# Performance work log

Measured on AMD Instinct MI355X. Metric: run time of the kernel, lower is better.

The kernel has to match this reference:

```python
import jax, jax.numpy as jnp
import numpy as np

D = 200          # in_feat == out_feat
N = 20000        # num nodes
E = 320000       # num edges
R = 512          # num relation types


def setup_inputs() -> dict:
    key = jax.random.key(0)
    ks = jax.random.split(key, 12)
    # glorot-ish init scale for params
    def glorot(k, shape):
        fan = shape[0] + shape[1]
        return jax.random.normal(k, shape, dtype=jnp.float32) * jnp.sqrt(2.0 / fan)
    return {
        "node": jax.random.normal(ks[0], (N, D), dtype=jnp.float32),
        "rel": jax.random.normal(ks[1], (R, D), dtype=jnp.float32),
        "norm": jax.random.uniform(ks[2], (N, 1), dtype=jnp.float32),
        "fre": jax.random.uniform(ks[3], (E,), dtype=jnp.float32),
        "w_triplet": glorot(ks[4], (3 * D, D)),
        "w_quad": glorot(ks[5], (D, D)),
        "loop_weight": glorot(ks[6], (D, D)),
        "evolve_loop_weight": glorot(ks[7], (D, D)),
        "edge_src": jax.random.randint(ks[8], (E,), 0, N, dtype=jnp.int64).astype(jnp.int32),
        "edge_dst": jax.random.randint(ks[9], (E,), 0, N, dtype=jnp.int64).astype(jnp.int32),
        "edge_type": jax.random.randint(ks[10], (E,), 0, R, dtype=jnp.int64).astype(jnp.int32),
    }


def reference(node, rel, norm, fre, w_triplet, w_quad, loop_weight,
              evolve_loop_weight, edge_src, edge_dst, edge_type):
    n = node.shape[0]
    d = node.shape[1]
    # gather per-edge features
    src_h = node[edge_src]            # [E, D]
    dst_h = node[edge_dst]            # [E, D]
    rel_emb = rel[edge_type]          # [E, D]
    # quads_msg_func: concat([src,rel,dst]) @ w_triplet, split to avoid [E,3D] concat
    W_s, W_r, W_d = w_triplet[:d], w_triplet[d:2 * d], w_triplet[2 * d:]
    triplet = src_h @ W_s + rel_emb @ W_r + dst_h @ W_d   # [E, D]
    a = (triplet + fre[:, None]) @ w_quad                 # [E, D]
    a = jax.nn.leaky_relu(a, negative_slope=0.01)
    # edge softmax over incoming edges per destination node (per channel)
    seg_max = jax.ops.segment_max(a, edge_dst, num_segments=n)   # [N, D]
    ex = jnp.exp(a - seg_max[edge_dst])
    seg_sum = jax.ops.segment_sum(ex, edge_dst, num_segments=n)  # [N, D]
    att = ex / seg_sum[edge_dst]
    # weighted message aggregation + per-node norm
    h = jax.ops.segment_sum(att * triplet, edge_dst, num_segments=n)
    h = h * norm
    # self-loop: loop_weight where in_degree > 0, else evolve_loop_weight
    deg = jax.ops.segment_sum(jnp.ones((edge_dst.shape[0],), dtype=jnp.float32),
                              edge_dst, num_segments=n)
    loop_msg = jnp.where((deg > 0)[:, None],
                         node @ loop_weight,
                         node @ evolve_loop_weight)
    return jax.nn.relu(h + loop_msg)
```

## Files before the change

### kernel.cpp

```cpp
#include <hip/hip_runtime.h>
#include <hip/hip_bf16.h>
#include <cstdint>
#include <cstddef>

#define DD 200
#define NN 20000
#define EE 320000
#define RRR 512
#define KP 256
#define KREAL 224
#define MT 157
#define NT 10
#define RMT 4
#define RNT 4
#define NBLK_NODE (MT * NT)

#define PB_NODE 10000
#define PB_REL  (PB_NODE + 256)
#define PB_HIST (PB_REL + 1250)
#define PB_W    (PB_HIST + 200)
#define PB_CQ   (PB_W + 1)
#define PB_PAD  (PB_CQ + 196)

typedef __attribute__((ext_vector_type(8))) short bf16x8;
typedef __attribute__((ext_vector_type(4))) float f32x4;

__device__ __forceinline__ float bf2f_lo(unsigned int u) { return __uint_as_float(u << 16); }
__device__ __forceinline__ float bf2f_hi(unsigned int u) { return __uint_as_float(u & 0xffff0000u); }
__device__ __forceinline__ unsigned short f2bf(float f) {
  unsigned int x = __float_as_uint(f);
  return (unsigned short)((x + 0x7fffu + ((x >> 16) & 1u)) >> 16);
}
__device__ __forceinline__ unsigned int f2bf2(float a, float b) {
  return (unsigned int)f2bf(a) | ((unsigned int)f2bf(b) << 16);
}
__device__ __forceinline__ void gl_lds16(const unsigned short* g, unsigned short* l) {
  __builtin_amdgcn_global_load_lds(
      (const __attribute__((address_space(1))) void*)g,
      (__attribute__((address_space(3))) void*)l, 16, 0, 0);
}

__global__ __launch_bounds__(256) void kPrep(const float* __restrict__ node, const float* __restrict__ rel,
                                             const int* __restrict__ dst,
                                             const float* __restrict__ wt, const float* __restrict__ wq,
                                             const float* __restrict__ lw, const float* __restrict__ elw,
                                             unsigned int* __restrict__ Au, unsigned int* __restrict__ Arelu,
                                             int* __restrict__ deg,
                                             unsigned short* __restrict__ Bt, unsigned short* __restrict__ BtRel,
                                             float* __restrict__ cq) {
  int b = blockIdx.x, t = threadIdx.x;
  if (b < PB_NODE) {
    int h = t >> 7, tt = t & 127;
    int n = b * 2 + h;
    unsigned v = 0;
    if (tt < 100) { float2 f = ((const float2*)(node + (size_t)n * DD))[tt]; v = f2bf2(f.x, f.y); }
    Au[(size_t)n * 128 + tt] = v;
  } else if (b < PB_REL) {
    int h = t >> 7, tt = t & 127;
    int r = (b - PB_NODE) * 2 + h;
    unsigned v = 0;
    if (tt < 100) { float2 f = ((const float2*)(rel + (size_t)r * DD))[tt]; v = f2bf2(f.x, f.y); }
    Arelu[(size_t)r * 128 + tt] = v;
  } else if (b < PB_HIST) {
    int e = (b - PB_REL) * 256 + t;
    if (e < EE) atomicAdd(&deg[dst[e]], 1);
  } else if (b < PB_W) {
    int k = b - PB_HIST, j = t;
    if (j >= DD) return;
    const float* w0 = wt + (size_t)k * DD;
    const float* w1 = wt + (size_t)(2 * DD + k) * DD;
    const float* w2 = wt + (size_t)(DD + k) * DD;
    float s0 = 0.f, s1 = 0.f, s2 = 0.f;
    for (int i = 0; i < DD; ++i) {
      float q = wq[i * DD + j];
      s0 = fmaf(w0[i], q, s0);
      s1 = fmaf(w1[i], q, s1);
      s2 = fmaf(w2[i], q, s2);
    }
    Bt[(2 * j) * KP + k]       = f2bf(w0[j]);
    Bt[(2 * j + 1) * KP + k]   = f2bf(s0);
    Bt[(400 + 2 * j) * KP + k] = f2bf(w1[j]);
    Bt[(401 + 2 * j) * KP + k] = f2bf(s1);
    Bt[(800 + 2 * j) * KP + k] = f2bf(lw[k * DD + j]);
    Bt[(801 + 2 * j) * KP + k] = f2bf(elw[k * DD + j]);
    BtRel[(2 * j) * KP + k]     = f2bf(w2[j]);
    BtRel[(2 * j + 1) * KP + k] = f2bf(s2);
  } else if (b < PB_CQ) {
    int j = t; if (j >= DD) return;
    float s = 0.f;
    for (int i = 0; i < DD; ++i) s += wq[i * DD + j];
    cq[j] = s;
  } else {
    int idx = (b - PB_CQ) * 256 + t;
    ((unsigned int*)Bt)[(idx / 28) * 128 + 100 + idx % 28] = 0;
  }
}

__global__ __launch_bounds__(1024) void k_scan(const int* __restrict__ deg, int* __restrict__ offs) {
  __shared__ int wsum[16];
  int tid = threadIdx.x, lane = tid & 63, wv = tid >> 6;
  const int4* deg4 = (const int4*)deg;
  int4* offs4 = (int4*)offs;
  int4 v[5]; int ps[5]; int tsum = 0;
#pragma unroll
  for (int c = 0; c < 5; ++c) {
    int idx = tid * 5 + c;
    v[c] = (idx < 5000) ? deg4[idx] : make_int4(0, 0, 0, 0);
    ps[c] = tsum;
    tsum += v[c].x + v[c].y + v[c].z + v[c].w;
  }
  int x = tsum;
#pragma unroll
  for (int off = 1; off < 64; off <<= 1) {
    int y = __shfl_up(x, off, 64);
    if (lane >= off) x += y;
  }
  if (lane == 63) wsum[wv] = x;
  __syncthreads();
  if (wv == 0) {
    int w = (lane < 16) ? wsum[lane] : 0;
#pragma unroll
    for (int off = 1; off < 16; off <<= 1) {
      int y = __shfl_up(w, off, 64);
      if (lane >= off) w += y;
    }
    if (lane < 16) wsum[lane] = w;
  }
  __syncthreads();
  int pre = ((wv > 0) ? wsum[wv - 1] : 0) + x - tsum;
#pragma unroll
  for (int c = 0; c < 5; ++c) {
    int idx = tid * 5 + c;
    if (idx < 5000) {
      int a = pre + ps[c];
      int bq = a + v[c].x, cc = bq + v[c].y, d = cc + v[c].z;
      offs4[idx] = make_int4(a, bq, cc, d);
    }
  }
  if (tid == 0) offs[NN] = wsum[15];
}

__global__ __launch_bounds__(256) void k_gemm(const unsigned short* __restrict__ A,
                                              const unsigned short* __restrict__ Bt,
                                              unsigned short* __restrict__ NT2u,
                                              const unsigned short* __restrict__ Arel,
                                              const unsigned short* __restrict__ BtRel,
                                              unsigned short* __restrict__ RelPu) {
  __shared__ unsigned short As[128 * 32];
  __shared__ unsigned short Bs[128 * 32];
  bool isrel = blockIdx.x >= NBLK_NODE;
  int bid, ntn;
  const unsigned short *Ag, *Bg;
  if (!isrel) { bid = blockIdx.x; ntn = NT; Ag = A; Bg = Bt; }
  else        { bid = blockIdx.x - NBLK_NODE; ntn = RNT; Ag = Arel; Bg = BtRel; }
  int mt = bid / ntn, nt = bid % ntn;
  int t = threadIdx.x, lane = t & 63, wv = t >> 6;
  int lr = lane & 15, k8 = lane >> 4;
  int wm = (wv >> 1) * 64, wn = (wv & 1) * 64;
  int sr = wv * 16 + (lane >> 2);
  int sc = lane & 3;
  f32x4 acc[4][4] = {};
  Ag += (size_t)(mt * 128) * KP;
  Bg += (size_t)(nt * 128) * KP;
  for (int kk = 0; kk < KREAL; kk += 32) {
#pragma unroll
    for (int i = 0; i < 2; ++i) {
      int row = i * 64 + sr;
      int gcol = kk + ((sc ^ (row & 3)) << 3);
      gl_lds16(Ag + (size_t)row * KP + gcol, As + i * 2048 + wv * 512);
      gl_lds16(Bg + (size_t)row * KP + gcol, Bs + i * 2048 + wv * 512);
    }
    __syncthreads();
    bf16x8 af[4], bfr[4];
#pragma unroll
    for (int mi = 0; mi < 4; ++mi) {
      int row = wm + mi * 16 + lr;
      af[mi] = *(const bf16x8*)(As + row * 32 + ((k8 ^ (row & 3)) << 3));
      int col = wn + mi * 16 + lr;
      bfr[mi] = *(const bf16x8*)(Bs + col * 32 + ((k8 ^ (col & 3)) << 3));
    }
#pragma unroll
    for (int mi = 0; mi < 4; ++mi)
#pragma unroll
      for (int ni = 0; ni < 4; ++ni)
        acc[mi][ni] = __builtin_amdgcn_mfma_f32_16x16x32_bf16(af[mi], bfr[ni], acc[mi][ni], 0, 0, 0);
    __syncthreads();
  }
  int rb = k8 * 4;
#pragma unroll
  for (int mi = 0; mi < 4; ++mi)
#pragma unroll
    for (int ni = 0; ni < 4; ++ni) {
      int col = nt * 128 + wn + ni * 16 + lr;
      if (!isrel) {
        if (col < 1200) {
          int g = col / 400, w = col - g * 400;
          unsigned short* dst = NT2u + (size_t)g * NN * 400 + w;
#pragma unroll
          for (int r = 0; r < 4; ++r) {
            int row = mt * 128 + wm + mi * 16 + rb + r;
            if (row < NN) dst[(size_t)row * 400] = f2bf(acc[mi][ni][r]);
          }
        }
      } else {
        if (col < 400) {
#pragma unroll
          for (int r = 0; r < 4; ++r) {
            int row = mt * 128 + wm + mi * 16 + rb + r;
            RelPu[(size_t)row * 400 + col] = f2bf(acc[mi][ni][r]);
          }
        }
      }
    }
}

__global__ __launch_bounds__(256) void k_scatter(const int* __restrict__ src, const int* __restrict__ dst,
                                                 const int* __restrict__ typ, const float* __restrict__ fre,
                                                 const int* __restrict__ offs, int* __restrict__ cursor,
                                                 int2* __restrict__ erec) {
  int e = blockIdx.x * 256 + threadIdx.x;
  if (e >= EE) return;
  int d = dst[e];
  int p = offs[d] + atomicAdd(&cursor[d], 1);
  erec[p] = make_int2(src[e] | (typ[e] << 15), __float_as_int(fre[e]));
}

__global__ __launch_bounds__(128) void k_agg(const uint2* __restrict__ GS2,
                                             const uint2* __restrict__ GD2,
                                             const uint2* __restrict__ GL2,
                                             const uint2* __restrict__ Rel2,
                                             const float2* __restrict__ cq2,
                                             const float* __restrict__ norm,
                                             const int* __restrict__ offs,
                                             const int2* __restrict__ erec,
                                             float* __restrict__ out) {
  int n = blockIdx.x;
  int j2 = threadIdx.x;
  if (j2 >= 100) return;
  int e0 = offs[n], e1 = offs[n + 1];
  uint2 dp = GD2[(size_t)n * 100 + j2];
  float xd0 = bf2f_lo(dp.x), xq0 = bf2f_hi(dp.x);
  float xd1 = bf2f_lo(dp.y), xq1 = bf2f_hi(dp.y);
  float2 cqv = cq2[j2];
  float s0 = 0.f, s1 = 0.f, num0 = 0.f, num1 = 0.f;
#define DO_EDGE(SP, RP, FI)                                                   \
  {                                                                           \
    float F = __int_as_float(FI);                                             \
    float t0 = bf2f_lo(SP.x) + bf2f_lo(RP.x);                                 \
    float a0 = bf2f_hi(SP.x) + bf2f_hi(RP.x) + fmaf(F, cqv.x, xq0);           \
    float t1 = bf2f_lo(SP.y) + bf2f_lo(RP.y);                                 \
    float a1 = bf2f_hi(SP.y) + bf2f_hi(RP.y) + fmaf(F, cqv.y, xq1);           \
    a0 = fmaxf(a0, 0.01f * a0); a1 = fmaxf(a1, 0.01f * a1);                   \
    float ev0 = __expf(a0), ev1 = __expf(a1);                                 \
    s0 += ev0; num0 = fmaf(ev0, t0, num0);                                    \
    s1 += ev1; num1 = fmaf(ev1, t1, num1);                                    \
  }
  int i = e0;
  for (; i + 8 <= e1; i += 8) {
    int2 r[8]; uint2 g[8], R[8];
#pragma unroll
    for (int u = 0; u < 8; ++u) r[u] = erec[i + u];
#pragma unroll
    for (int u = 0; u < 8; ++u) g[u] = GS2[((unsigned)r[u].x & 0x7fffu) * 100u + j2];
#pragma unroll
    for (int u = 0; u < 8; ++u) R[u] = Rel2[((unsigned)r[u].x >> 15) * 100u + j2];
#pragma unroll
    for (int u = 0; u < 8; ++u) DO_EDGE(g[u], R[u], r[u].y)
  }
  if (i + 4 <= e1) {
    int2 r[4]; uint2 g[4], R[4];
#pragma unroll
    for (int u = 0; u < 4; ++u) r[u] = erec[i + u];
#pragma unroll
    for (int u = 0; u < 4; ++u) g[u] = GS2[((unsigned)r[u].x & 0x7fffu) * 100u + j2];
#pragma unroll
    for (int u = 0; u < 4; ++u) R[u] = Rel2[((unsigned)r[u].x >> 15) * 100u + j2];
#pragma unroll
    for (int u = 0; u < 4; ++u) DO_EDGE(g[u], R[u], r[u].y)
    i += 4;
  }
  for (; i < e1; ++i) {
    int2 r = erec[i];
    uint2 g = GS2[((unsigned)r.x & 0x7fffu) * 100u + j2];
    uint2 R = Rel2[((unsigned)r.x >> 15) * 100u + j2];
    DO_EDGE(g, R, r.y)
  }
#undef DO_EDGE
  uint2 lp = GL2[(size_t)n * 100 + j2];
  float o0, o1;
  if (e1 > e0) {
    float nm = norm[n];
    o0 = (num0 / s0 + xd0) * nm + bf2f_lo(lp.x);
    o1 = (num1 / s1 + xd1) * nm + bf2f_lo(lp.y);
  } else {
    o0 = bf2f_hi(lp.x);
    o1 = bf2f_hi(lp.y);
  }
  ((float2*)(out + (size_t)n * DD))[j2] = make_float2(fmaxf(o0, 0.f), fmaxf(o1, 0.f));
}

extern "C" void kernel_launch(void* const* d_in, const int* in_sizes, int n_in,
                              void* d_out, int out_size, void* d_ws, size_t ws_size,
                              hipStream_t stream) {
  const float* node = (const float*)d_in[0];
  const float* rel  = (const float*)d_in[1];
  const float* norm = (const float*)d_in[2];
  const float* fre  = (const float*)d_in[3];
  const float* wt   = (const float*)d_in[4];
  const float* wq   = (const float*)d_in[5];
  const float* lw   = (const float*)d_in[6];
  const float* elw  = (const float*)d_in[7];
  const int* esrc = (const int*)d_in[8];
  const int* edst = (const int*)d_in[9];
  const int* etyp = (const int*)d_in[10];
  float* out = (float*)d_out;

  char* p = (char*)d_ws;
  auto carve = [&](size_t bytes) -> char* {
    char* r = p; p += (bytes + 255) & ~(size_t)255; return r;
  };
  unsigned short* A     = (unsigned short*)carve((size_t)(MT * 128) * KP * 2);
  unsigned short* Arel  = (unsigned short*)carve((size_t)RRR * KP * 2);
  unsigned short* BtAll = (unsigned short*)carve((size_t)(1280 + 512) * KP * 2);
  unsigned short* NT2   = (unsigned short*)carve((size_t)3 * NN * 400 * 2);
  unsigned short* RelP  = (unsigned short*)carve((size_t)RRR * 400 * 2);
  float* cq   = (float*)carve((size_t)DD * 4);
  int* degcur = (int*)carve((size_t)2 * NN * 4);
  int* offs   = (int*)carve((size_t)(NN + 1) * 4);
  int2* erec  = (int2*)carve((size_t)EE * 8);

  unsigned short* Bt    = BtAll;
  unsigned short* BtRel = BtAll + (size_t)1280 * KP;
  int* deg    = degcur;
  int* cursor = degcur + NN;

  const uint2* GS2 = (const uint2*)NT2;
  const uint2* GD2 = GS2 + (size_t)NN * 100;
  const uint2* GL2 = GS2 + (size_t)2 * NN * 100;

  hipMemsetAsync(degcur, 0, (size_t)2 * NN * 4, stream);
  kPrep<<<PB_PAD, 256, 0, stream>>>(node, rel, edst, wt, wq, lw, elw,
                                    (unsigned int*)A, (unsigned int*)Arel, deg, Bt, BtRel, cq);
  k_scan<<<1, 1024, 0, stream>>>(deg, offs);
  k_scatter<<<(EE + 255) / 256, 256, 0, stream>>>(esrc, edst, etyp, fre, offs, cursor, erec);
  k_gemm<<<NBLK_NODE + RMT * RNT, 256, 0, stream>>>(A, Bt, NT2, Arel, BtRel, RelP);
  k_agg<<<NN, 128, 0, stream>>>(GS2, GD2, GL2, (const uint2*)RelP, (const float2*)cq,
                                norm, offs, erec, out);
}
```

Baseline: 142.3 us.

## Merge scatter into GEMM launch, software-pipeline edge loads, fold log2e into weights

Moves the edge-scatter blocks into the same launch as the bf16 GEMM, so CSR record building overlaps with the matrix work and one kernel launch goes away. The log2(e) factor is folded into the attention-logit weight columns and cq, so the aggregation kernel can call exp2f instead of __expf. The per-node edge loop becomes a double-buffered 4-edge pipeline that issues the next batch's gathers before computing the current batch, replacing the 8-wide unroll. Risks are extra register pressure in k_agg, and a small precision change because the scale is applied before rounding to bf16.

```diff
diff --git a/kernel.cpp b/kernel.cpp
--- a/kernel.cpp
+++ b/kernel.cpp
@@ -14,6 +14,9 @@
 #define RMT 4
 #define RNT 4
 #define NBLK_NODE (MT * NT)
+#define NBLK_GEMM (NBLK_NODE + RMT * RNT)
+#define NBLK_SCAT ((EE + 255) / 256)
+#define LOG2E 1.4426950408889634f
 
 #define PB_NODE 10000
 #define PB_REL  (PB_NODE + 256)
@@ -78,18 +81,18 @@
       s2 = fmaf(w2[i], q, s2);
     }
     Bt[(2 * j) * KP + k]       = f2bf(w0[j]);
-    Bt[(2 * j + 1) * KP + k]   = f2bf(s0);
+    Bt[(2 * j + 1) * KP + k]   = f2bf(s0 * LOG2E);
     Bt[(400 + 2 * j) * KP + k] = f2bf(w1[j]);
-    Bt[(401 + 2 * j) * KP + k] = f2bf(s1);
+    Bt[(401 + 2 * j) * KP + k] = f2bf(s1 * LOG2E);
     Bt[(800 + 2 * j) * KP + k] = f2bf(lw[k * DD + j]);
     Bt[(801 + 2 * j) * KP + k] = f2bf(elw[k * DD + j]);
     BtRel[(2 * j) * KP + k]     = f2bf(w2[j]);
-    BtRel[(2 * j + 1) * KP + k] = f2bf(s2);
+    BtRel[(2 * j + 1) * KP + k] = f2bf(s2 * LOG2E);
   } else if (b < PB_CQ) {
     int j = t; if (j >= DD) return;
     float s = 0.f;
     for (int i = 0; i < DD; ++i) s += wq[i * DD + j];
-    cq[j] = s;
+    cq[j] = s * LOG2E;
   } else {
     int idx = (b - PB_CQ) * 256 + t;
     ((unsigned int*)Bt)[(idx / 28) * 128 + 100 + idx % 28] = 0;
@@ -140,14 +143,26 @@
   if (tid == 0) offs[NN] = wsum[15];
 }
 
-__global__ __launch_bounds__(256) void k_gemm(const unsigned short* __restrict__ A,
-                                              const unsigned short* __restrict__ Bt,
-                                              unsigned short* __restrict__ NT2u,
-                                              const unsigned short* __restrict__ Arel,
-                                              const unsigned short* __restrict__ BtRel,
-                                              unsigned short* __restrict__ RelPu) {
+__global__ __launch_bounds__(256) void k_gs(const unsigned short* __restrict__ A,
+                                            const unsigned short* __restrict__ Bt,
+                                            unsigned short* __restrict__ NT2u,
+                                            const unsigned short* __restrict__ Arel,
+                                            const unsigned short* __restrict__ BtRel,
+                                            unsigned short* __restrict__ RelPu,
+                                            const int* __restrict__ esrc, const int* __restrict__ edst,
+                                            const int* __restrict__ etyp, const float* __restrict__ fre,
+                                            const int* __restrict__ offs, int* __restrict__ cursor,
+                                            int2* __restrict__ erec) {
   __shared__ unsigned short As[128 * 32];
   __shared__ unsigned short Bs[128 * 32];
+  if (blockIdx.x >= NBLK_GEMM) {
+    int e = (blockIdx.x - NBLK_GEMM) * 256 + threadIdx.x;
+    if (e >= EE) return;
+    int d = edst[e];
+    int p = offs[d] + atomicAdd(&cursor[d], 1);
+    erec[p] = make_int2(esrc[e] | (etyp[e] << 15), __float_as_int(fre[e]));
+    return;
+  }
   bool isrel = blockIdx.x >= NBLK_NODE;
   int bid, ntn;
   const unsigned short *Ag, *Bg;
@@ -212,17 +227,6 @@
         }
       }
     }
-}
-
-__global__ __launch_bounds__(256) void k_scatter(const int* __restrict__ src, const int* __restrict__ dst,
-                                                 const int* __restrict__ typ, const float* __restrict__ fre,
-                                                 const int* __restrict__ offs, int* __restrict__ cursor,
-                                                 int2* __restrict__ erec) {
-  int e = blockIdx.x * 256 + threadIdx.x;
-  if (e >= EE) return;
-  int d = dst[e];
-  int p = offs[d] + atomicAdd(&cursor[d], 1);
-  erec[p] = make_int2(src[e] | (typ[e] << 15), __float_as_int(fre[e]));
 }
 
 __global__ __launch_bounds__(128) void k_agg(const uint2* __restrict__ GS2,
@@ -251,40 +255,51 @@
     float t1 = bf2f_lo(SP.y) + bf2f_lo(RP.y);                                 \
     float a1 = bf2f_hi(SP.y) + bf2f_hi(RP.y) + fmaf(F, cqv.y, xq1);           \
     a0 = fmaxf(a0, 0.01f * a0); a1 = fmaxf(a1, 0.01f * a1);                   \
-    float ev0 = __expf(a0), ev1 = __expf(a1);                                 \
+    float ev0 = exp2f(a0), ev1 = exp2f(a1);                                   \
     s0 += ev0; num0 = fmaf(ev0, t0, num0);                                    \
     s1 += ev1; num1 = fmaf(ev1, t1, num1);                                    \
   }
-  int i = e0;
-  for (; i + 8 <= e1; i += 8) {
-    int2 r[8]; uint2 g[8], R[8];
-#pragma unroll
-    for (int u = 0; u < 8; ++u) r[u] = erec[i + u];
-#pragma unroll
-    for (int u = 0; u < 8; ++u) g[u] = GS2[((unsigned)r[u].x & 0x7fffu) * 100u + j2];
-#pragma unroll
-    for (int u = 0; u < 8; ++u) R[u] = Rel2[((unsigned)r[u].x >> 15) * 100u + j2];
-#pragma unroll
-    for (int u = 0; u < 8; ++u) DO_EDGE(g[u], R[u], r[u].y)
-  }
-  if (i + 4 <= e1) {
-    int2 r[4]; uint2 g[4], R[4];
-#pragma unroll
-    for (int u = 0; u < 4; ++u) r[u] = erec[i + u];
-#pragma unroll
-    for (int u = 0; u < 4; ++u) g[u] = GS2[((unsigned)r[u].x & 0x7fffu) * 100u + j2];
-#pragma unroll
-    for (int u = 0; u < 4; ++u) R[u] = Rel2[((unsigned)r[u].x >> 15) * 100u + j2];
-#pragma unroll
-    for (int u = 0; u < 4; ++u) DO_EDGE(g[u], R[u], r[u].y)
-    i += 4;
-  }
-  for (; i < e1; ++i) {
+#define LOADB(R, GS, GR, base)                                                \
+  {                                                                           \
+    _Pragma("unroll")                                                         \
+    for (int u = 0; u < 4; ++u) R[u] = erec[(base) + u];                      \
+    _Pragma("unroll")                                                         \
+    for (int u = 0; u < 4; ++u) GS[u] = GS2[((unsigned)R[u].x & 0x7fffu) * 100u + j2]; \
+    _Pragma("unroll")                                                         \
+    for (int u = 0; u < 4; ++u) GR[u] = Rel2[((unsigned)R[u].x >> 15) * 100u + j2];    \
+  }
+#define COMPB(R, GS, GR)                                                      \
+  {                                                                           \
+    _Pragma("unroll")                                                         \
+    for (int u = 0; u < 4; ++u) DO_EDGE(GS[u], GR[u], R[u].y)                 \
+  }
+  int cnt = e1 - e0;
+  int nb = cnt >> 2;
+  int2 rA[4], rB[4];
+  uint2 gsA[4], grA[4], gsB[4], grB[4];
+  if (nb > 0) LOADB(rA, gsA, grA, e0)
+  int b = 1;
+  for (; b + 1 < nb; b += 2) {
+    LOADB(rB, gsB, grB, e0 + b * 4)
+    COMPB(rA, gsA, grA)
+    LOADB(rA, gsA, grA, e0 + (b + 1) * 4)
+    COMPB(rB, gsB, grB)
+  }
+  if (b < nb) {
+    LOADB(rB, gsB, grB, e0 + b * 4)
+    COMPB(rA, gsA, grA)
+    COMPB(rB, gsB, grB)
+  } else if (nb > 0) {
+    COMPB(rA, gsA, grA)
+  }
+  for (int i = e0 + nb * 4; i < e1; ++i) {
     int2 r = erec[i];
     uint2 g = GS2[((unsigned)r.x & 0x7fffu) * 100u + j2];
     uint2 R = Rel2[((unsigned)r.x >> 15) * 100u + j2];
     DO_EDGE(g, R, r.y)
   }
+#undef COMPB
+#undef LOADB
 #undef DO_EDGE
   uint2 lp = GL2[(size_t)n * 100 + j2];
   float o0, o1;
@@ -342,8 +357,8 @@
   kPrep<<<PB_PAD, 256, 0, stream>>>(node, rel, edst, wt, wq, lw, elw,
                                     (unsigned int*)A, (unsigned int*)Arel, deg, Bt, BtRel, cq);
   k_scan<<<1, 1024, 0, stream>>>(deg, offs);
-  k_scatter<<<(EE + 255) / 256, 256, 0, stream>>>(esrc, edst, etyp, fre, offs, cursor, erec);
-  k_gemm<<<NBLK_NODE + RMT * RNT, 256, 0, stream>>>(A, Bt, NT2, Arel, BtRel, RelP);
+  k_gs<<<NBLK_GEMM + NBLK_SCAT, 256, 0, stream>>>(A, Bt, NT2, Arel, BtRel, RelP,
+                                                  esrc, edst, etyp, fre, offs, cursor, erec);
   k_agg<<<NN, 128, 0, stream>>>(GS2, GD2, GL2, (const uint2*)RelP, (const float2*)cq,
                                 norm, offs, erec, out);
 }
```

Result: faster. 134.2 us (-5.7%).
